# Kernel tuning notes

Measured on AMD Instinct MI355X. Metric: run time of the kernel, lower is better.

## Reference

```python
import jax, jax.numpy as jnp
import numpy as np

B, S, H, NH, L, V, P = 2, 1024, 768, 12, 4, 32000, 1024
HD = H // NH  # head dim = 64; matches scale_val = hidden/num_heads


def setup_inputs() -> dict:
    key = jax.random.key(0)
    ks = jax.random.split(key, 18)
    sc = 0.02
    n = jax.random.normal
    return {
        "input_ids": jax.random.randint(ks[0], (B, S), 0, V, dtype=jnp.int32),
        "seq_mask": jnp.ones((B, S), jnp.float32),
        "bpe_emb": (n(ks[1], (V, H)) * sc).astype(jnp.float32),
        "pos_emb": (n(ks[2], (P, H)) * sc).astype(jnp.float32),
        "qkv_w": (n(ks[3], (L, H, 3 * H)) * sc).astype(jnp.float32),
        "qkv_b": jnp.zeros((L, 3 * H), jnp.float32),
        "res_w": (n(ks[4], (L, H, H)) * sc).astype(jnp.float32),
        "res_b": jnp.zeros((L, H), jnp.float32),
        "ln1_g": jnp.ones((L, H), jnp.float32),
        "ln1_b": jnp.zeros((L, H), jnp.float32),
        "ff1_w": (n(ks[5], (L, H, 4 * H)) * sc).astype(jnp.float32),
        "ff1_b": jnp.zeros((L, 4 * H), jnp.float32),
        "ff2_w": (n(ks[6], (L, 4 * H, H)) * sc).astype(jnp.float32),
        "ff2_b": jnp.zeros((L, H), jnp.float32),
        "ln2_g": jnp.ones((L, H), jnp.float32),
        "ln2_b": jnp.zeros((L, H), jnp.float32),
        "pred_w": (n(ks[7], (H, V)) * sc).astype(jnp.float32),
    }


def _layer_norm(x, g, b, e=1e-5):
    u = jnp.mean(x, -1, keepdims=True)
    s = jnp.mean((x - u) ** 2, -1, keepdims=True)
    return g * ((x - u) / jnp.sqrt(s + e)) + b


def _attention(x, seq_mask, w_qkv, b_qkv, w_res, b_res):
    qkv = x @ w_qkv + b_qkv                    # [B,S,3H]
    q, k, v = jnp.split(qkv, 3, axis=-1)
    q = q.reshape(B, S, NH, HD)
    k = k.reshape(B, S, NH, HD)
    v = v.reshape(B, S, NH, HD)
    score = jnp.einsum('bqhd,bkhd->bhqk', q, k) / jnp.sqrt(jnp.float32(HD))
    tril = jnp.tril(jnp.ones((S, S), jnp.float32))           # causal
    mask = tril[None, None] * seq_mask[:, None, None, :]      # [B,1,S,S]
    score = score + (1.0 - mask) * -1e9
    prob = jax.nn.softmax(score, axis=-1)      # dropout rate 0 -> identity
    val = jnp.einsum('bhqk,bkhd->bqhd', prob, v).reshape(B, S, H)
    return val @ w_res + b_res                 # dropout rate 0 -> identity


def reference(input_ids, seq_mask, bpe_emb, pos_emb, qkv_w, qkv_b, res_w, res_b,
              ln1_g, ln1_b, ff1_w, ff1_b, ff2_w, ff2_b, ln2_g, ln2_b, pred_w):
    pos_idx = jnp.arange(S)
    h = bpe_emb[input_ids] + pos_emb[pos_idx][None]           # [B,S,H]
    for l in range(L):
        a = _attention(h, seq_mask, qkv_w[l], qkv_b[l], res_w[l], res_b[l])
        h = _layer_norm(h + a, ln1_g[l], ln1_b[l])
        m = (jax.nn.gelu(h @ ff1_w[l] + ff1_b[l], approximate=False)
             @ ff2_w[l] + ff2_b[l])
        h = _layer_norm(h + m, ln2_g[l], ln2_b[l])
    pred_score = h @ pred_w                                   # [B,S,V]
    pred_prob = jax.nn.softmax(pred_score, axis=-1)
    return pred_score, pred_prob
```

## Files before the change

### kernel.cpp

```cpp
#include <hip/hip_runtime.h>
#include <math.h>

#define BB 2
#define SS 1024
#define HH 768
#define NHEAD 12
#define HDIM 64
#define NLAYER 4
#define VV 32000
#define MROWS (BB*SS)

typedef unsigned short u16;
typedef __attribute__((ext_vector_type(8))) short short8;
typedef __attribute__((ext_vector_type(4))) float f32x4;
typedef __attribute__((ext_vector_type(4))) unsigned short u16x4;

__device__ __forceinline__ u16 f2bf(float f) {
    union { float f; unsigned u; } x; x.f = f;
    unsigned r = (x.u + 0x7fff + ((x.u >> 16) & 1)) >> 16;
    return (u16)r;
}
__device__ __forceinline__ float bf2f(u16 b) {
    union { unsigned u; float f; } x; x.u = ((unsigned)b) << 16;
    return x.f;
}

__device__ __forceinline__ void gload_lds16(const u16* g, u16* l) {
    __builtin_amdgcn_global_load_lds((const __attribute__((address_space(1))) void*)g,
                                     (__attribute__((address_space(3))) void*)l, 16, 0, 0);
}

__global__ __launch_bounds__(256) void conv_transpose(
    const float* __restrict__ W, u16* __restrict__ Wt, int K, int N) {
    int l = blockIdx.z;
    W  += (size_t)l * K * N;
    Wt += (size_t)l * K * N;
    __shared__ u16 tile[32][33];
    int k0 = blockIdx.y * 32, n0 = blockIdx.x * 32;
    int t = threadIdx.x;
    int ky = t >> 3, nx = (t & 7) * 4;
    float4 v = *(const float4*)(W + (size_t)(k0 + ky) * N + n0 + nx);
    tile[nx + 0][ky] = f2bf(v.x);
    tile[nx + 1][ky] = f2bf(v.y);
    tile[nx + 2][ky] = f2bf(v.z);
    tile[nx + 3][ky] = f2bf(v.w);
    __syncthreads();
    int nr = t >> 3, kc = (t & 7) * 4;
    u16x4 o;
    o[0] = tile[nr][kc + 0]; o[1] = tile[nr][kc + 1];
    o[2] = tile[nr][kc + 2]; o[3] = tile[nr][kc + 3];
    *(u16x4*)(Wt + (size_t)(n0 + nr) * K + k0 + kc) = o;
}

__global__ void embed_kernel(const int* __restrict__ ids,
                             const float* __restrict__ bpe,
                             const float* __restrict__ pos,
                             float* __restrict__ h, u16* __restrict__ hb) {
    int row = blockIdx.x;
    int s = row % SS;
    int id = ids[row];
    const float4* br = (const float4*)(bpe + (size_t)id * HH);
    const float4* pr = (const float4*)(pos + (size_t)s * HH);
    float4* hr = (float4*)(h + (size_t)row * HH);
    u16x4* hbr = (u16x4*)(hb + (size_t)row * HH);
    int t = threadIdx.x;
    float4 a = br[t], c = pr[t];
    a.x += c.x; a.y += c.y; a.z += c.z; a.w += c.w;
    hr[t] = a;
    u16x4 u; u[0] = f2bf(a.x); u[1] = f2bf(a.y); u[2] = f2bf(a.z); u[3] = f2bf(a.w);
    hbr[t] = u;
}

template<int BM, int ACT, int WF32, int WBF>
__global__ __launch_bounds__(256) void mfma_gemm(
    const u16* __restrict__ A, const u16* __restrict__ Wt,
    const float* __restrict__ bias, float* __restrict__ C,
    u16* __restrict__ Cb, int M, int N, int K) {
    constexpr int MR = BM / 32;
    __shared__ u16 As[2 * BM * 64];
    __shared__ u16 Bs[2 * 128 * 64];
    const int tid = threadIdx.x;
    const int lane = tid & 63;
    const int wid = tid >> 6;

    const int nwg = gridDim.x * gridDim.y;
    int id = blockIdx.x + gridDim.x * blockIdx.y;
    int id2 = (nwg & 7) ? id : ((id & 7) * (nwg >> 3) + (id >> 3));
    const int brow = (id2 % gridDim.x) * BM;
    const int bcol = (id2 / gridDim.x) * 128;

    const int wr = (wid >> 1) * (BM / 2);
    const int wc = (wid & 1) * 64;
    f32x4 acc[MR][4] = {};

    const u16* Abase = A + (size_t)brow * K;
    const u16* Bbase = Wt + (size_t)bcol * K;
    const int lrow = lane & 15;
    const int lhi = lane >> 4;

    auto stage = [&](u16* Ad, u16* Bd, int kt) {
#pragma unroll
        for (int c0 = 0; c0 < BM * 8; c0 += 256) {
            int c = c0 + tid;
            int r = c >> 3, s = c & 7;
            gload_lds16(Abase + (size_t)r * K + kt + ((s ^ (r & 7)) * 8), Ad + c * 8);
        }
#pragma unroll
        for (int c0 = 0; c0 < 1024; c0 += 256) {
            int c = c0 + tid;
            int r = c >> 3, s = c & 7;
            gload_lds16(Bbase + (size_t)r * K + kt + ((s ^ (r & 7)) * 8), Bd + c * 8);
        }
    };

    const int nt = K / 64;
    stage(As, Bs, 0);
    for (int t = 0; t < nt; ++t) {
        u16* Ac = As + (t & 1) * (BM * 64);
        u16* Bc = Bs + (t & 1) * (128 * 64);
        if (t + 1 < nt) {
            stage(As + ((t + 1) & 1) * (BM * 64),
                  Bs + ((t + 1) & 1) * (128 * 64), (t + 1) * 64);
            if constexpr (BM == 128) asm volatile("s_waitcnt vmcnt(8)" ::: "memory");
            else                     asm volatile("s_waitcnt vmcnt(6)" ::: "memory");
        } else {
            asm volatile("s_waitcnt vmcnt(0)" ::: "memory");
        }
        __builtin_amdgcn_s_barrier();
        __builtin_amdgcn_sched_barrier(0);

        short8 a[MR][2], b[4][2];
#pragma unroll
        for (int m = 0; m < MR; ++m) {
            const int R = wr + m * 16 + lrow;
            char* rp = (char*)Ac + R * 128;
#pragma unroll
            for (int kk = 0; kk < 2; ++kk)
                a[m][kk] = *(const short8*)(rp + (((kk * 4 + lhi) ^ (R & 7)) * 16));
        }
#pragma unroll
        for (int n = 0; n < 4; ++n) {
            const int R = wc + n * 16 + lrow;
            char* rp = (char*)Bc + R * 128;
#pragma unroll
            for (int kk = 0; kk < 2; ++kk)
                b[n][kk] = *(const short8*)(rp + (((kk * 4 + lhi) ^ (R & 7)) * 16));
        }
        __builtin_amdgcn_s_setprio(1);
#pragma unroll
        for (int kk = 0; kk < 2; ++kk)
#pragma unroll
            for (int m = 0; m < MR; ++m)
#pragma unroll
                for (int n = 0; n < 4; ++n)
                    acc[m][n] = __builtin_amdgcn_mfma_f32_16x16x32_bf16(a[m][kk], b[n][kk], acc[m][n], 0, 0, 0);
        __builtin_amdgcn_s_setprio(0);

        __builtin_amdgcn_sched_barrier(0);
        __builtin_amdgcn_s_barrier();
    }

    const int lr4 = (lane >> 4) * 4;
#pragma unroll
    for (int n = 0; n < 4; ++n) {
        int col = bcol + wc + n * 16 + lrow;
        float bv = bias ? bias[col] : 0.f;
#pragma unroll
        for (int m = 0; m < MR; ++m) {
#pragma unroll
            for (int j = 0; j < 4; ++j) {
                int row = brow + wr + m * 16 + lr4 + j;
                float v = acc[m][n][j] + bv;
                if (ACT == 1) v = 0.5f * v * (1.f + erff(v * 0.70710678118654752f));
                if (WF32) C[(size_t)row * N + col] = v;
                if (WBF)  Cb[(size_t)row * N + col] = f2bf(v);
            }
        }
    }
}

__global__ __launch_bounds__(256) void attn_kernel(
    const u16* __restrict__ qkvb, const float* __restrict__ seq_mask,
    u16* __restrict__ av) {
    __shared__ u16 Ks[64 * 64];
    __shared__ u16 Vt[64 * 64];
    __shared__ u16 Ps[64 * 64];
    const int qb = gridDim.x - 1 - blockIdx.x;
    const int hd = blockIdx.y, b = blockIdx.z;
    const int t = threadIdx.x;
    const int lane = t & 63;
    const int w = t >> 6;
    const int lrow = lane & 15;
    const int lhi = lane >> 4;
    const int q0 = qb * 64;
    const size_t rs = 3 * HH;

    short8 aq[2];
    {
        const u16* qrow = qkvb + (size_t)(b * SS + q0 + w * 16 + lrow) * rs + hd * HDIM;
        aq[0] = *(const short8*)(qrow + lhi * 8);
        aq[1] = *(const short8*)(qrow + 32 + lhi * 8);
    }

    f32x4 o[4] = {};
    float m_[4] = {-INFINITY, -INFINITY, -INFINITY, -INFINITY};
    float l_[4] = {0.f, 0.f, 0.f, 0.f};

    const int kr = t >> 2, dc = t & 3;
    short8 kA, kB, vA, vB;
    {
        const u16* kbase = qkvb + (size_t)(b * SS + kr) * rs + HH + hd * HDIM + dc * 16;
        kA = *(const short8*)(kbase);
        kB = *(const short8*)(kbase + 8);
        vA = *(const short8*)(kbase + HH);
        vB = *(const short8*)(kbase + HH + 8);
    }

    for (int kt = 0; kt <= qb; ++kt) {
        const int k0 = kt * 64;
        __syncthreads();
        {
            char* krowp = (char*)Ks + kr * 128;
            *(short8*)(krowp + (((dc * 32 + 0)  ^ ((kr & 7) << 4)))) = kA;
            *(short8*)(krowp + (((dc * 32 + 16) ^ ((kr & 7) << 4)))) = kB;
#pragma unroll
            for (int e = 0; e < 8; ++e) {
                int d0 = dc * 16 + e;
                int d1 = dc * 16 + 8 + e;
                *(u16*)((char*)Vt + d0 * 128 + ((kr * 2) ^ ((d0 & 7) << 4))) = (u16)vA[e];
                *(u16*)((char*)Vt + d1 * 128 + ((kr * 2) ^ ((d1 & 7) << 4))) = (u16)vB[e];
            }
        }
        __syncthreads();

        if (kt < qb) {
            const u16* kbase = qkvb + (size_t)(b * SS + k0 + 64 + kr) * rs + HH + hd * HDIM + dc * 16;
            kA = *(const short8*)(kbase);
            kB = *(const short8*)(kbase + 8);
            vA = *(const short8*)(kbase + HH);
            vB = *(const short8*)(kbase + HH + 8);
        }

        f32x4 s[4] = {};
        __builtin_amdgcn_s_setprio(1);
#pragma unroll
        for (int n = 0; n < 4; ++n) {
            const int krow = n * 16 + lrow;
            char* kp = (char*)Ks + krow * 128;
#pragma unroll
            for (int c = 0; c < 2; ++c) {
                short8 bk = *(const short8*)(kp + ((c * 64 + lhi * 16) ^ ((krow & 7) << 4)));
                s[n] = __builtin_amdgcn_mfma_f32_16x16x32_bf16(aq[c], bk, s[n], 0, 0, 0);
            }
        }
        __builtin_amdgcn_s_setprio(0);

        float sm[4];
#pragma unroll
        for (int n = 0; n < 4; ++n) sm[n] = seq_mask[b * SS + k0 + n * 16 + lrow];
        const int diag = (kt == qb);
#pragma unroll
        for (int j = 0; j < 4; ++j) {
            const int qglob = q0 + w * 16 + lhi * 4 + j;
            float sv[4];
#pragma unroll
            for (int n = 0; n < 4; ++n) {
                const int kglob = k0 + n * 16 + lrow;
                float msk = (diag && kglob > qglob) ? 0.f : sm[n];
                sv[n] = s[n][j] * 0.125f + (1.f - msk) * (-1e9f);
            }
            float tm = fmaxf(fmaxf(sv[0], sv[1]), fmaxf(sv[2], sv[3]));
            tm = fmaxf(tm, __shfl_xor(tm, 1));
            tm = fmaxf(tm, __shfl_xor(tm, 2));
            tm = fmaxf(tm, __shfl_xor(tm, 4));
            tm = fmaxf(tm, __shfl_xor(tm, 8));
            float mn = fmaxf(m_[j], tm);
            float sc = __expf(m_[j] - mn);
            float ps = 0.f;
#pragma unroll
            for (int n = 0; n < 4; ++n) {
                float p = __expf(sv[n] - mn);
                s[n][j] = p;
                ps += p;
            }
            ps += __shfl_xor(ps, 1);
            ps += __shfl_xor(ps, 2);
            ps += __shfl_xor(ps, 4);
            ps += __shfl_xor(ps, 8);
            l_[j] = l_[j] * sc + ps;
            m_[j] = mn;
#pragma unroll
            for (int dn = 0; dn < 4; ++dn) o[dn][j] *= sc;
        }

#pragma unroll
        for (int j = 0; j < 4; ++j) {
            const int prow = w * 16 + lhi * 4 + j;
            char* pp = (char*)Ps + prow * 128;
#pragma unroll
            for (int n = 0; n < 4; ++n)
                *(u16*)(pp + ((n * 32 + lrow * 2) ^ ((prow & 7) << 4))) = f2bf(s[n][j]);
        }

        const int arow = w * 16 + lrow;
        char* ap_p = (char*)Ps + arow * 128;
        __builtin_amdgcn_s_setprio(1);
#pragma unroll
        for (int c = 0; c < 2; ++c) {
            short8 ap = *(const short8*)(ap_p + ((c * 64 + lhi * 16) ^ ((arow & 7) << 4)));
#pragma unroll
            for (int dn = 0; dn < 4; ++dn) {
                const int vrow = dn * 16 + lrow;
                short8 bv = *(const short8*)((char*)Vt + vrow * 128 +
                                             ((c * 64 + lhi * 16) ^ ((vrow & 7) << 4)));
                o[dn] = __builtin_amdgcn_mfma_f32_16x16x32_bf16(ap, bv, o[dn], 0, 0, 0);
            }
        }
        __builtin_amdgcn_s_setprio(0);
    }

#pragma unroll
    for (int j = 0; j < 4; ++j) {
        const int q = q0 + w * 16 + lhi * 4 + j;
        const float inv = 1.f / l_[j];
        u16* orow = av + (size_t)(b * SS + q) * HH + hd * HDIM;
#pragma unroll
        for (int dn = 0; dn < 4; ++dn)
            orow[dn * 16 + lrow] = f2bf(o[dn][j] * inv);
    }
}

__global__ void add_ln_kernel(float* __restrict__ h, u16* __restrict__ hb,
                              const float* __restrict__ a,
                              const float* __restrict__ g,
                              const float* __restrict__ bta) {
    int row = blockIdx.x;
    int t = threadIdx.x;
    __shared__ float red[256];
    size_t base = (size_t)row * HH;
    float x0 = h[base + t]       + a[base + t];
    float x1 = h[base + t + 256] + a[base + t + 256];
    float x2 = h[base + t + 512] + a[base + t + 512];

    red[t] = x0 + x1 + x2;
    __syncthreads();
    for (int o = 128; o; o >>= 1) { if (t < o) red[t] += red[t + o]; __syncthreads(); }
    float mean = red[0] * (1.0f / 768.0f);
    __syncthreads();

    float d0 = x0 - mean, d1 = x1 - mean, d2 = x2 - mean;
    red[t] = d0 * d0 + d1 * d1 + d2 * d2;
    __syncthreads();
    for (int o = 128; o; o >>= 1) { if (t < o) red[t] += red[t + o]; __syncthreads(); }
    float var = red[0] * (1.0f / 768.0f);
    float inv = 1.0f / sqrtf(var + 1e-5f);

    float y0 = g[t]       * d0 * inv + bta[t];
    float y1 = g[t + 256] * d1 * inv + bta[t + 256];
    float y2 = g[t + 512] * d2 * inv + bta[t + 512];
    h[base + t] = y0;       hb[base + t] = f2bf(y0);
    h[base + t + 256] = y1; hb[base + t + 256] = f2bf(y1);
    h[base + t + 512] = y2; hb[base + t + 512] = f2bf(y2);
}

__global__ __launch_bounds__(512) void softmax_v_kernel(
    const float* __restrict__ score, float* __restrict__ prob) {
    __shared__ u16 srow[VV];
    __shared__ float red[512];
    int row = blockIdx.x;
    int t = threadIdx.x;
    const float4* sr = (const float4*)(score + (size_t)row * VV);
    float4* pr = (float4*)(prob + (size_t)row * VV);
    const int n4 = VV / 4;

    float mx = -INFINITY;
    for (int i = t; i < n4; i += 512) {
        float4 v = sr[i];
        u16x4 u; u[0] = f2bf(v.x); u[1] = f2bf(v.y); u[2] = f2bf(v.z); u[3] = f2bf(v.w);
        *(u16x4*)(srow + i * 4) = u;
        mx = fmaxf(mx, fmaxf(fmaxf(bf2f(u[0]), bf2f(u[1])), fmaxf(bf2f(u[2]), bf2f(u[3]))));
    }
    red[t] = mx; __syncthreads();
    for (int o = 256; o; o >>= 1) { if (t < o) red[t] = fmaxf(red[t], red[t + o]); __syncthreads(); }
    mx = red[0];
    __syncthreads();

    float s = 0.f;
    for (int i = t; i < n4; i += 512) {
        u16x4 u = *(const u16x4*)(srow + i * 4);
        s += __expf(bf2f(u[0]) - mx) + __expf(bf2f(u[1]) - mx)
           + __expf(bf2f(u[2]) - mx) + __expf(bf2f(u[3]) - mx);
    }
    red[t] = s; __syncthreads();
    for (int o = 256; o; o >>= 1) { if (t < o) red[t] += red[t + o]; __syncthreads(); }
    float inv = 1.0f / red[0];

    for (int i = t; i < n4; i += 512) {
        u16x4 u = *(const u16x4*)(srow + i * 4);
        float4 o4;
        o4.x = __expf(bf2f(u[0]) - mx) * inv; o4.y = __expf(bf2f(u[1]) - mx) * inv;
        o4.z = __expf(bf2f(u[2]) - mx) * inv; o4.w = __expf(bf2f(u[3]) - mx) * inv;
        pr[i] = o4;
    }
}

extern "C" void kernel_launch(void* const* d_in, const int* in_sizes, int n_in,
                              void* d_out, int out_size, void* d_ws, size_t ws_size,
                              hipStream_t stream) {
    const int*   ids      = (const int*)d_in[0];
    const float* seq_mask = (const float*)d_in[1];
    const float* bpe      = (const float*)d_in[2];
    const float* pos      = (const float*)d_in[3];
    const float* qkv_w    = (const float*)d_in[4];
    const float* qkv_b    = (const float*)d_in[5];
    const float* res_w    = (const float*)d_in[6];
    const float* res_b    = (const float*)d_in[7];
    const float* ln1_g    = (const float*)d_in[8];
    const float* ln1_b    = (const float*)d_in[9];
    const float* ff1_w    = (const float*)d_in[10];
    const float* ff1_b    = (const float*)d_in[11];
    const float* ff2_w    = (const float*)d_in[12];
    const float* ff2_b    = (const float*)d_in[13];
    const float* ln2_g    = (const float*)d_in[14];
    const float* ln2_b    = (const float*)d_in[15];
    const float* pred_w   = (const float*)d_in[16];

    float* out_score = (float*)d_out;
    float* out_prob  = out_score + (size_t)MROWS * VV;

    size_t off = 0;
    auto take = [&](size_t bytes) -> size_t {
        size_t p = off; off += (bytes + 255) & ~(size_t)255; return p;
    };
    const size_t o_qkvT = take((size_t)NLAYER * HH * 3 * HH * 2);
    const size_t o_resT = take((size_t)NLAYER * HH * HH * 2);
    const size_t o_ff1T = take((size_t)NLAYER * HH * 4 * HH * 2);
    const size_t o_ff2T = take((size_t)NLAYER * 4 * HH * HH * 2);
    const size_t o_predT = take((size_t)HH * VV * 2);
    const size_t o_h    = take((size_t)MROWS * HH * 4);
    const size_t o_a    = take((size_t)MROWS * HH * 4);
    const size_t o_qkvb = take((size_t)MROWS * 3 * HH * 2);
    const size_t o_hb   = take((size_t)MROWS * HH * 2);
    const size_t o_avb  = take((size_t)MROWS * HH * 2);
    const size_t o_midb = take((size_t)MROWS * 4 * HH * 2);
    const size_t need = off;

    char* arena = (ws_size >= need) ? (char*)d_ws : (char*)out_prob;
    u16*   qkvT = (u16*)(arena + o_qkvT);
    u16*   resT = (u16*)(arena + o_resT);
    u16*   ff1T = (u16*)(arena + o_ff1T);
    u16*   ff2T = (u16*)(arena + o_ff2T);
    u16*   predT = (u16*)(arena + o_predT);
    float* h    = (float*)(arena + o_h);
    float* a    = (float*)(arena + o_a);
    u16*   qkvb = (u16*)(arena + o_qkvb);
    u16*   hb   = (u16*)(arena + o_hb);
    u16*   avb  = (u16*)(arena + o_avb);
    u16*   midb = (u16*)(arena + o_midb);

    conv_transpose<<<dim3(3 * HH / 32, HH / 32, NLAYER), 256, 0, stream>>>(qkv_w, qkvT, HH, 3 * HH);
    conv_transpose<<<dim3(HH / 32, HH / 32, NLAYER), 256, 0, stream>>>(res_w, resT, HH, HH);
    conv_transpose<<<dim3(4 * HH / 32, HH / 32, NLAYER), 256, 0, stream>>>(ff1_w, ff1T, HH, 4 * HH);
    conv_transpose<<<dim3(HH / 32, 4 * HH / 32, NLAYER), 256, 0, stream>>>(ff2_w, ff2T, 4 * HH, HH);
    conv_transpose<<<dim3(VV / 32, HH / 32, 1), 256, 0, stream>>>(pred_w, predT, HH, VV);

    embed_kernel<<<MROWS, 192, 0, stream>>>(ids, bpe, pos, h, hb);

    for (int l = 0; l < NLAYER; ++l) {
        mfma_gemm<128, 0, 0, 1><<<dim3(MROWS / 128, 3 * HH / 128), 256, 0, stream>>>(
            hb, qkvT + (size_t)l * HH * 3 * HH, qkv_b + (size_t)l * 3 * HH,
            nullptr, qkvb, MROWS, 3 * HH, HH);
        attn_kernel<<<dim3(SS / 64, NHEAD, BB), 256, 0, stream>>>(qkvb, seq_mask, avb);
        mfma_gemm<64, 0, 1, 0><<<dim3(MROWS / 64, HH / 128), 256, 0, stream>>>(
            avb, resT + (size_t)l * HH * HH, res_b + (size_t)l * HH,
            a, nullptr, MROWS, HH, HH);
        add_ln_kernel<<<MROWS, 256, 0, stream>>>(h, hb, a,
            ln1_g + (size_t)l * HH, ln1_b + (size_t)l * HH);
        mfma_gemm<128, 1, 0, 1><<<dim3(MROWS / 128, 4 * HH / 128), 256, 0, stream>>>(
            hb, ff1T + (size_t)l * HH * 4 * HH, ff1_b + (size_t)l * 4 * HH,
            nullptr, midb, MROWS, 4 * HH, HH);
        mfma_gemm<64, 0, 1, 0><<<dim3(MROWS / 64, HH / 128), 256, 0, stream>>>(
            midb, ff2T + (size_t)l * 4 * HH * HH, ff2_b + (size_t)l * HH,
            a, nullptr, MROWS, HH, 4 * HH);
        add_ln_kernel<<<MROWS, 256, 0, stream>>>(h, hb, a,
            ln2_g + (size_t)l * HH, ln2_b + (size_t)l * HH);
    }

    mfma_gemm<128, 0, 1, 0><<<dim3(MROWS / 128, VV / 128), 256, 0, stream>>>(
        hb, predT, nullptr, out_score, nullptr, MROWS, VV, HH);
    softmax_v_kernel<<<MROWS, 512, 0, stream>>>(out_score, out_prob);
}
```

Before: 1.032 ms.

## Split causal attention KV range in two with combine kernel; widen vocab GEMM tile

The attention kernel now splits each query block's causal key range into two halves, handled by separate workgroups. Each half writes unnormalized fp32 partial outputs plus running max and sum, and a new combine kernel merges them into the bf16 attention output. This doubles the attention grid to improve load balance and occupancy, at the cost of extra fp32 partial traffic and one more launch per layer. Separately, the vocabulary projection GEMM uses a 256-row tile with 512 threads to get more reuse of weight tiles, which needs larger LDS.

```diff
diff --git a/kernel.cpp b/kernel.cpp
--- a/kernel.cpp
+++ b/kernel.cpp
@@ -72,11 +72,12 @@
 }
 
 template<int BM, int ACT, int WF32, int WBF>
-__global__ __launch_bounds__(256) void mfma_gemm(
+__global__ __launch_bounds__(BM == 256 ? 512 : 256) void mfma_gemm(
     const u16* __restrict__ A, const u16* __restrict__ Wt,
     const float* __restrict__ bias, float* __restrict__ C,
     u16* __restrict__ Cb, int M, int N, int K) {
-    constexpr int MR = BM / 32;
+    constexpr int T = (BM == 256) ? 512 : 256;
+    constexpr int MR = (BM >= 128) ? 4 : 2;
     __shared__ u16 As[2 * BM * 64];
     __shared__ u16 Bs[2 * 128 * 64];
     const int tid = threadIdx.x;
@@ -89,7 +90,7 @@
     const int brow = (id2 % gridDim.x) * BM;
     const int bcol = (id2 / gridDim.x) * 128;
 
-    const int wr = (wid >> 1) * (BM / 2);
+    const int wr = (wid >> 1) * (MR * 16);
     const int wc = (wid & 1) * 64;
     f32x4 acc[MR][4] = {};
 
@@ -100,13 +101,13 @@
 
     auto stage = [&](u16* Ad, u16* Bd, int kt) {
 #pragma unroll
-        for (int c0 = 0; c0 < BM * 8; c0 += 256) {
+        for (int c0 = 0; c0 < BM * 8; c0 += T) {
             int c = c0 + tid;
             int r = c >> 3, s = c & 7;
             gload_lds16(Abase + (size_t)r * K + kt + ((s ^ (r & 7)) * 8), Ad + c * 8);
         }
 #pragma unroll
-        for (int c0 = 0; c0 < 1024; c0 += 256) {
+        for (int c0 = 0; c0 < 1024; c0 += T) {
             int c = c0 + tid;
             int r = c >> 3, s = c & 7;
             gload_lds16(Bbase + (size_t)r * K + kt + ((s ^ (r & 7)) * 8), Bd + c * 8);
@@ -121,8 +122,8 @@
         if (t + 1 < nt) {
             stage(As + ((t + 1) & 1) * (BM * 64),
                   Bs + ((t + 1) & 1) * (128 * 64), (t + 1) * 64);
-            if constexpr (BM == 128) asm volatile("s_waitcnt vmcnt(8)" ::: "memory");
-            else                     asm volatile("s_waitcnt vmcnt(6)" ::: "memory");
+            if constexpr (BM == 128)      asm volatile("s_waitcnt vmcnt(8)" ::: "memory");
+            else                          asm volatile("s_waitcnt vmcnt(6)" ::: "memory");
         } else {
             asm volatile("s_waitcnt vmcnt(0)" ::: "memory");
         }
@@ -181,11 +182,12 @@
 
 __global__ __launch_bounds__(256) void attn_kernel(
     const u16* __restrict__ qkvb, const float* __restrict__ seq_mask,
-    u16* __restrict__ av) {
+    float* __restrict__ Opart, float2* __restrict__ ml) {
     __shared__ u16 Ks[64 * 64];
     __shared__ u16 Vt[64 * 64];
     __shared__ u16 Ps[64 * 64];
-    const int qb = gridDim.x - 1 - blockIdx.x;
+    const int qb = (gridDim.x / 2) - 1 - (blockIdx.x >> 1);
+    const int sp = blockIdx.x & 1;
     const int hd = blockIdx.y, b = blockIdx.z;
     const int t = threadIdx.x;
     const int lane = t & 63;
@@ -195,6 +197,11 @@
     const int q0 = qb * 64;
     const size_t rs = 3 * HH;
 
+    const int ntile = qb + 1;
+    const int half = (ntile + 1) >> 1;
+    const int kbeg = sp ? half : 0;
+    const int kend = sp ? ntile : half;
+
     short8 aq[2];
     {
         const u16* qrow = qkvb + (size_t)(b * SS + q0 + w * 16 + lrow) * rs + hd * HDIM;
@@ -208,15 +215,15 @@
 
     const int kr = t >> 2, dc = t & 3;
     short8 kA, kB, vA, vB;
-    {
-        const u16* kbase = qkvb + (size_t)(b * SS + kr) * rs + HH + hd * HDIM + dc * 16;
+    if (kbeg < kend) {
+        const u16* kbase = qkvb + (size_t)(b * SS + kbeg * 64 + kr) * rs + HH + hd * HDIM + dc * 16;
         kA = *(const short8*)(kbase);
         kB = *(const short8*)(kbase + 8);
         vA = *(const short8*)(kbase + HH);
         vB = *(const short8*)(kbase + HH + 8);
     }
 
-    for (int kt = 0; kt <= qb; ++kt) {
+    for (int kt = kbeg; kt < kend; ++kt) {
         const int k0 = kt * 64;
         __syncthreads();
         {
@@ -233,7 +240,7 @@
         }
         __syncthreads();
 
-        if (kt < qb) {
+        if (kt + 1 < kend) {
             const u16* kbase = qkvb + (size_t)(b * SS + k0 + 64 + kr) * rs + HH + hd * HDIM + dc * 16;
             kA = *(const short8*)(kbase);
             kB = *(const short8*)(kbase + 8);
@@ -319,15 +326,35 @@
         __builtin_amdgcn_s_setprio(0);
     }
 
+    float* obase = Opart + (size_t)sp * MROWS * HH;
 #pragma unroll
     for (int j = 0; j < 4; ++j) {
         const int q = q0 + w * 16 + lhi * 4 + j;
-        const float inv = 1.f / l_[j];
-        u16* orow = av + (size_t)(b * SS + q) * HH + hd * HDIM;
+        float* orow = obase + (size_t)(b * SS + q) * HH + hd * HDIM;
 #pragma unroll
         for (int dn = 0; dn < 4; ++dn)
-            orow[dn * 16 + lrow] = f2bf(o[dn][j] * inv);
-    }
+            orow[dn * 16 + lrow] = o[dn][j];
+        if (lrow == 0) {
+            float2 v; v.x = m_[j]; v.y = l_[j];
+            ml[((size_t)sp * MROWS + b * SS + q) * NHEAD + hd] = v;
+        }
+    }
+}
+
+__global__ __launch_bounds__(768) void attn_combine(
+    const float* __restrict__ Opart, const float2* __restrict__ ml,
+    u16* __restrict__ av) {
+    const int row = blockIdx.x;
+    const int t = threadIdx.x;
+    const int hd = t >> 6;
+    float2 a1 = ml[(size_t)row * NHEAD + hd];
+    float2 a2 = ml[((size_t)MROWS + row) * NHEAD + hd];
+    float m = fmaxf(a1.x, a2.x);
+    float c1 = __expf(a1.x - m), c2 = __expf(a2.x - m);
+    float inv = 1.f / (a1.y * c1 + a2.y * c2);
+    float o1 = Opart[(size_t)row * HH + t];
+    float o2 = Opart[(size_t)(MROWS + row) * HH + t];
+    av[(size_t)row * HH + t] = f2bf((o1 * c1 + o2 * c2) * inv);
 }
 
 __global__ void add_ln_kernel(float* __restrict__ h, u16* __restrict__ hb,
@@ -443,6 +470,8 @@
     const size_t o_hb   = take((size_t)MROWS * HH * 2);
     const size_t o_avb  = take((size_t)MROWS * HH * 2);
     const size_t o_midb = take((size_t)MROWS * 4 * HH * 2);
+    const size_t o_op   = take((size_t)2 * MROWS * HH * 4);
+    const size_t o_ml   = take((size_t)2 * MROWS * NHEAD * 8);
     const size_t need = off;
 
     char* arena = (ws_size >= need) ? (char*)d_ws : (char*)out_prob;
@@ -457,6 +486,8 @@
     u16*   hb   = (u16*)(arena + o_hb);
     u16*   avb  = (u16*)(arena + o_avb);
     u16*   midb = (u16*)(arena + o_midb);
+    float* opart = (float*)(arena + o_op);
+    float2* mlb  = (float2*)(arena + o_ml);
 
     conv_transpose<<<dim3(3 * HH / 32, HH / 32, NLAYER), 256, 0, stream>>>(qkv_w, qkvT, HH, 3 * HH);
     conv_transpose<<<dim3(HH / 32, HH / 32, NLAYER), 256, 0, stream>>>(res_w, resT, HH, HH);
@@ -470,7 +501,8 @@
         mfma_gemm<128, 0, 0, 1><<<dim3(MROWS / 128, 3 * HH / 128), 256, 0, stream>>>(
             hb, qkvT + (size_t)l * HH * 3 * HH, qkv_b + (size_t)l * 3 * HH,
             nullptr, qkvb, MROWS, 3 * HH, HH);
-        attn_kernel<<<dim3(SS / 64, NHEAD, BB), 256, 0, stream>>>(qkvb, seq_mask, avb);
+        attn_kernel<<<dim3(SS / 64 * 2, NHEAD, BB), 256, 0, stream>>>(qkvb, seq_mask, opart, mlb);
+        attn_combine<<<MROWS, 768, 0, stream>>>(opart, mlb, avb);
         mfma_gemm<64, 0, 1, 0><<<dim3(MROWS / 64, HH / 128), 256, 0, stream>>>(
             avb, resT + (size_t)l * HH * HH, res_b + (size_t)l * HH,
             a, nullptr, MROWS, HH, HH);
@@ -486,7 +518,7 @@
             ln2_g + (size_t)l * HH, ln2_b + (size_t)l * HH);
     }
 
-    mfma_gemm<128, 0, 1, 0><<<dim3(MROWS / 128, VV / 128), 256, 0, stream>>>(
+    mfma_gemm<256, 0, 1, 0><<<dim3(MROWS / 256, VV / 128), 512, 0, stream>>>(
         hb, predT, nullptr, out_score, nullptr, MROWS, VV, HH);
     softmax_v_kernel<<<MROWS, 512, 0, stream>>>(out_score, out_prob);
 }
```

Result: no change. 1.046 ms (+1.3%).
